# Kernel optimization log

Hardware: AMD Instinct MI355X
Metric: run time of the kernel (lower is better)

The kernel has to match this reference:

```python
import jax, jax.numpy as jnp
import numpy as np

B, T, D, H, S, Ms = 16, 512, 64, 128, 100, 20  # batch, time, input, controller, slots, slot width


def setup_inputs() -> dict:
    key = jax.random.key(0)
    ks = jax.random.split(key, 12)
    rn = lambda k, shape, s=0.08: (jax.random.normal(k, shape, dtype=jnp.float32) * s)
    inp = {}
    inp["inputs"] = jax.random.normal(ks[0], (B, T, D), dtype=jnp.float32)
    inp["memory"] = jax.random.normal(ks[1], (S, Ms), dtype=jnp.float32)
    # Keras LSTM params (gate order i, f, c, o)
    inp["lstm_kernel"] = rn(ks[2], (D, 4 * H))
    inp["lstm_rkernel"] = rn(ks[3], (H, 4 * H))
    inp["lstm_bias"] = jnp.zeros((4 * H,), jnp.float32)
    # 2 read heads: key Dense(H -> Ms)
    inp["read_Wk"] = rn(ks[4], (2, H, Ms)); inp["read_bk"] = jnp.zeros((2, Ms), jnp.float32)
    # 2 write heads: key / erase(sigmoid) / add Dense(H -> Ms)
    inp["write_Wk"] = rn(ks[5], (2, H, Ms)); inp["write_bk"] = jnp.zeros((2, Ms), jnp.float32)
    inp["write_We"] = rn(ks[6], (2, H, Ms)); inp["write_be"] = jnp.zeros((2, Ms), jnp.float32)
    inp["write_Wa"] = rn(ks[7], (2, H, Ms)); inp["write_ba"] = jnp.zeros((2, Ms), jnp.float32)
    return inp


def _lstm(x, Wk, Rk, b):
    # x: [B,T,D] -> h_seq: [B,T,H]; Keras gate order i,f,c,o
    xw = jnp.einsum('btd,dh->bth', x, Wk) + b  # precompute input projection
    h0 = jnp.zeros((x.shape[0], Rk.shape[0]), x.dtype)
    c0 = jnp.zeros_like(h0)

    def step(carry, xt):
        h, c = carry
        z = xt + h @ Rk  # [B,4H]
        i, f, g, o = jnp.split(z, 4, axis=-1)
        i = jax.nn.sigmoid(i); f = jax.nn.sigmoid(f)
        g = jnp.tanh(g); o = jax.nn.sigmoid(o)
        c = f * c + i * g
        h = o * jnp.tanh(c)
        return (h, c), h

    _, hs = jax.lax.scan(step, (h0, c0), jnp.swapaxes(xw, 0, 1))
    return jnp.swapaxes(hs, 0, 1)


def _l2n(x):
    # tf.nn.l2_normalize semantics with epsilon 1e-12
    return x / jnp.sqrt(jnp.maximum(jnp.sum(x * x, axis=-1, keepdims=True), 1e-12))


def _neg_cos(a, b):
    # tf.keras.losses.cosine_similarity returns NEGATIVE cosine
    return -jnp.sum(_l2n(a) * _l2n(b), axis=-1)


def reference(inputs, memory, lstm_kernel, lstm_rkernel, lstm_bias,
              read_Wk, read_bk, write_Wk, write_bk,
              write_We, write_be, write_Wa, write_ba):
    ctrl = _lstm(inputs, lstm_kernel, lstm_rkernel, lstm_bias)  # [B,T,H]

    # content-addressable reads (on pre-write memory, as in original)
    reads = []
    for i in range(2):
        k = jax.nn.softmax(jnp.einsum('bth,hm->btm', ctrl, read_Wk[i]) + read_bk[i], axis=-1)
        sim = _neg_cos(k[:, :, None, :], memory[None, None, :, :])  # [B,T,S]
        w = jax.nn.softmax(sim, axis=-1)
        reads.append(jnp.einsum('bts,sm->btm', w, memory))

    # content-addressable erase/add writes, applied per (batch, time) position
    mem = memory[None, None, :, :]  # broadcast to [B,T,S,Ms] lazily
    for i in range(2):
        k = jax.nn.softmax(jnp.einsum('bth,hm->btm', ctrl, write_Wk[i]) + write_bk[i], axis=-1)
        sim = _neg_cos(k[:, :, None, :], mem)  # [B,T,S]
        w = jax.nn.softmax(sim, axis=-1)
        e = jax.nn.sigmoid(jnp.einsum('bth,hm->btm', ctrl, write_We[i]) + write_be[i])
        a = jnp.einsum('bth,hm->btm', ctrl, write_Wa[i]) + write_ba[i]
        mem = (1.0 - w[..., None] * e[:, :, None, :]) * mem + w[..., None] * a[:, :, None, :]

    out = jnp.concatenate([ctrl] + reads, axis=-1)  # [B,T,H+2*Ms]
    return out, mem
```

## Files before the change

### kernel.cpp

```cpp
#include <hip/hip_runtime.h>
#include <hip/hip_bf16.h>

#define BB 16
#define TT 512
#define DD 64
#define HH 128
#define SS 100
#define MSZ 20
#define NROW (BB*TT)
#define FOURH 512

typedef __attribute__((ext_vector_type(8))) short bh8;
typedef __attribute__((ext_vector_type(4))) float fv4;

__device__ __forceinline__ float frcp(float x){ return __builtin_amdgcn_rcpf(x); }
__device__ __forceinline__ float sigmoidf_(float x){
    return frcp(1.0f + __expf(-x));
}
__device__ __forceinline__ float tanhf_(float x){
    float t = __expf(2.0f * x);
    return 1.0f - 2.0f * frcp(t + 1.0f);
}
__device__ __forceinline__ unsigned short f2bf(float f){
    __hip_bfloat16 h = __float2bfloat16(f);
    union { __hip_bfloat16 b; unsigned short u; } cv; cv.b = h;
    return cv.u;
}

__device__ __forceinline__ void lds_sync(){
    asm volatile("s_waitcnt lgkmcnt(0)" ::: "memory");
    __builtin_amdgcn_s_barrier();
    __builtin_amdgcn_sched_barrier(0);
}

__global__ __launch_bounds__(512) void k_xw(const float* __restrict__ inp,
        const float* __restrict__ Wk, const float* __restrict__ bias,
        float* __restrict__ xw){
    __shared__ float in_s[8 * DD];
    int tid = threadIdx.x;
    int r0 = blockIdx.x * 8;
    in_s[tid] = inp[(size_t)r0 * DD + tid];
    __syncthreads();
    int j = tid;
    int n = j & 127, g = j >> 7;
    float wreg[DD];
    #pragma unroll
    for (int d = 0; d < DD; ++d) wreg[d] = Wk[d * FOURH + j];
    float bv = bias[j];
    const float4* in4 = reinterpret_cast<const float4*>(in_s);
    #pragma unroll
    for (int r = 0; r < 8; ++r){
        float acc = bv;
        #pragma unroll
        for (int q = 0; q < DD/4; ++q){
            float4 iv = in4[r*(DD/4) + q];
            acc = fmaf(iv.x, wreg[4*q+0], acc);
            acc = fmaf(iv.y, wreg[4*q+1], acc);
            acc = fmaf(iv.z, wreg[4*q+2], acc);
            acc = fmaf(iv.w, wreg[4*q+3], acc);
        }
        xw[(size_t)(r0 + r) * FOURH + n*4 + g] = acc;
    }
}

__global__ __launch_bounds__(512, 2) void k_scan(const float* __restrict__ xw,
        const float* __restrict__ Rk, float* __restrict__ ctrl){
    __shared__ __align__(16) unsigned short hbuf0[HH];
    __shared__ __align__(16) unsigned short hbuf1[HH];
    const int tid = threadIdx.x;
    const int b  = blockIdx.x;
    const int w  = tid >> 6;
    const int l  = tid & 63;
    const int q  = l >> 4;
    const int lo = l & 15;
    if (tid < HH){ hbuf0[tid] = 0; hbuf1[tid] = 0; }
    bh8 bf[4][4];
    #pragma unroll
    for (int Ti = 0; Ti < 4; ++Ti){
        const int col = Ti*128 + w*16 + lo;
        #pragma unroll
        for (int kk = 0; kk < 4; ++kk){
            union { unsigned short us[8]; bh8 v; } u;
            #pragma unroll
            for (int j = 0; j < 8; ++j)
                u.us[j] = f2bf(Rk[(size_t)(kk*32 + q*8 + j)*FOURH + col]);
            bf[Ti][kk] = u.v;
        }
    }
    const bool upd = (q == 0);
    const bool rdh = (lo == 0);
    const int  n   = w*16 + lo;
    const float4* xb4 = reinterpret_cast<const float4*>(xw) + (size_t)b*TT*HH + n;
    float* cptr = ctrl + (size_t)b*TT*HH + n;
    float c0 = 0.0f;
    float4 x0 = {0,0,0,0}, x1 = {0,0,0,0}, xp0 = {0,0,0,0}, xp1 = {0,0,0,0};
    if (upd){ x0 = xb4[0]; x1 = xb4[(size_t)HH]; }
    union AU { uint4 u; bh8 v; };
    AU a0, a1, a2, a3;
    a0.u = make_uint4(0u,0u,0u,0u); a1.u = a0.u; a2.u = a0.u; a3.u = a0.u;
    const fv4 zz = {0.f, 0.f, 0.f, 0.f};
    __syncthreads();

#define MFMA16() \
        fv4 z0 = __builtin_amdgcn_mfma_f32_16x16x32_bf16(a0.v, bf[0][0], zz, 0,0,0); \
        fv4 z1 = __builtin_amdgcn_mfma_f32_16x16x32_bf16(a0.v, bf[1][0], zz, 0,0,0); \
        fv4 z2 = __builtin_amdgcn_mfma_f32_16x16x32_bf16(a0.v, bf[2][0], zz, 0,0,0); \
        fv4 z3 = __builtin_amdgcn_mfma_f32_16x16x32_bf16(a0.v, bf[3][0], zz, 0,0,0); \
        z0 = __builtin_amdgcn_mfma_f32_16x16x32_bf16(a1.v, bf[0][1], z0, 0,0,0); \
        z1 = __builtin_amdgcn_mfma_f32_16x16x32_bf16(a1.v, bf[1][1], z1, 0,0,0); \
        z2 = __builtin_amdgcn_mfma_f32_16x16x32_bf16(a1.v, bf[2][1], z2, 0,0,0); \
        z3 = __builtin_amdgcn_mfma_f32_16x16x32_bf16(a1.v, bf[3][1], z3, 0,0,0); \
        z0 = __builtin_amdgcn_mfma_f32_16x16x32_bf16(a2.v, bf[0][2], z0, 0,0,0); \
        z1 = __builtin_amdgcn_mfma_f32_16x16x32_bf16(a2.v, bf[1][2], z1, 0,0,0); \
        z2 = __builtin_amdgcn_mfma_f32_16x16x32_bf16(a2.v, bf[2][2], z2, 0,0,0); \
        z3 = __builtin_amdgcn_mfma_f32_16x16x32_bf16(a2.v, bf[3][2], z3, 0,0,0); \
        z0 = __builtin_amdgcn_mfma_f32_16x16x32_bf16(a3.v, bf[0][3], z0, 0,0,0); \
        z1 = __builtin_amdgcn_mfma_f32_16x16x32_bf16(a3.v, bf[1][3], z1, 0,0,0); \
        z2 = __builtin_amdgcn_mfma_f32_16x16x32_bf16(a3.v, bf[2][3], z2, 0,0,0); \
        z3 = __builtin_amdgcn_mfma_f32_16x16x32_bf16(a3.v, bf[3][3], z3, 0,0,0);

    for (int t = 0; t < TT; t += 2){
        if (rdh){
            const uint4* hr = reinterpret_cast<const uint4*>(hbuf0);
            a0.u = hr[q]; a1.u = hr[q+4]; a2.u = hr[q+8]; a3.u = hr[q+12];
        }
        {
            const int tn = (t+2 < TT) ? t+2 : TT-1;
            if (upd) xp0 = xb4[(size_t)tn * HH];
        }
        {
            MFMA16();
            if (upd){
                float ig = sigmoidf_(z0[0] + x0.x);
                float fg = sigmoidf_(z1[0] + x0.y);
                float gg = tanhf_   (z2[0] + x0.z);
                float og = sigmoidf_(z3[0] + x0.w);
                c0 = fg * c0 + ig * gg;
                float h = og * tanhf_(c0);
                cptr[(size_t)t * HH] = h;
                hbuf1[n] = f2bf(h);
            }
        }
        lds_sync();
        if (rdh){
            const uint4* hr = reinterpret_cast<const uint4*>(hbuf1);
            a0.u = hr[q]; a1.u = hr[q+4]; a2.u = hr[q+8]; a3.u = hr[q+12];
        }
        {
            const int tn = (t+3 < TT) ? t+3 : TT-1;
            if (upd) xp1 = xb4[(size_t)tn * HH];
        }
        {
            MFMA16();
            if (upd){
                float ig = sigmoidf_(z0[0] + x1.x);
                float fg = sigmoidf_(z1[0] + x1.y);
                float gg = tanhf_   (z2[0] + x1.z);
                float og = sigmoidf_(z3[0] + x1.w);
                c0 = fg * c0 + ig * gg;
                float h = og * tanhf_(c0);
                cptr[(size_t)(t+1) * HH] = h;
                hbuf0[n] = f2bf(h);
            }
        }
        x0 = xp0; x1 = xp1;
        lds_sync();
    }
#undef MFMA16
}

__device__ __forceinline__ float blocksum128(float v, float* red){
    #pragma unroll
    for (int o = 1; o < 64; o <<= 1) v += __shfl_xor(v, o, 64);
    int tid = threadIdx.x;
    if ((tid & 63) == 0) red[tid >> 6] = v;
    __syncthreads();
    float s = red[0] + red[1];
    __syncthreads();
    return s;
}

__global__ __launch_bounds__(128) void k_heads(const float* __restrict__ ctrl,
        const float* __restrict__ memory,
        const float* __restrict__ rWk, const float* __restrict__ rbk,
        const float* __restrict__ wWk, const float* __restrict__ wbk,
        const float* __restrict__ wWe, const float* __restrict__ wbe,
        const float* __restrict__ wWa, const float* __restrict__ wba,
        float* __restrict__ out, float* __restrict__ outmem){
    __shared__ float mem0[SS * MSZ];
    __shared__ float cs[HH];
    __shared__ float rn[SS];
    __shared__ float khat[4][MSZ];
    __shared__ float ea[4][MSZ];
    __shared__ float wrd[2][SS];
    __shared__ float red[2];
    __shared__ float pz[160];
    int tid = threadIdx.x;
    int bt = blockIdx.x;
    for (int idx = tid; idx < SS * MSZ; idx += 128) mem0[idx] = memory[idx];
    if (tid < HH){
        float v = ctrl[(size_t)bt * HH + tid];
        cs[tid] = v;
        out[(size_t)bt * 168 + tid] = v;
    }
    __syncthreads();
    if (tid < SS){
        float s2 = 0.0f;
        #pragma unroll
        for (int m = 0; m < MSZ; ++m){ float v = mem0[tid*MSZ + m]; s2 = fmaf(v, v, s2); }
        rn[tid] = rsqrtf(fmaxf(s2, 1e-12f));
    }
    for (int j = tid; j < 160; j += 128){
        int p = j / MSZ, m = j % MSZ;
        const float* Wp; const float* bp;
        switch (p){
            case 0:  Wp = rWk;            bp = rbk;        break;
            case 1:  Wp = rWk + HH*MSZ;   bp = rbk + MSZ;  break;
            case 2:  Wp = wWk;            bp = wbk;        break;
            case 3:  Wp = wWk + HH*MSZ;   bp = wbk + MSZ;  break;
            case 4:  Wp = wWe;            bp = wbe;        break;
            case 5:  Wp = wWe + HH*MSZ;   bp = wbe + MSZ;  break;
            case 6:  Wp = wWa;            bp = wba;        break;
            default: Wp = wWa + HH*MSZ;   bp = wba + MSZ;  break;
        }
        float acc = bp[m];
        const float* wcol = Wp + m;
        #pragma unroll 16
        for (int k = 0; k < HH; ++k)
            acc = fmaf(cs[k], wcol[k*MSZ], acc);
        pz[j] = acc;
    }
    __syncthreads();
    {
        int g = tid >> 5, lm = tid & 31;
        float z = (lm < MSZ) ? pz[g*MSZ + lm] : 0.0f;
        float e = (lm < MSZ) ? __expf(z) : 0.0f;
        float ssum = e;
        #pragma unroll
        for (int o = 1; o < 32; o <<= 1) ssum += __shfl_xor(ssum, o, 32);
        float kv = e / ssum;
        float qs = kv * kv;
        #pragma unroll
        for (int o = 1; o < 32; o <<= 1) qs += __shfl_xor(qs, o, 32);
        float kn = kv * rsqrtf(fmaxf(qs, 1e-12f));
        if (lm < MSZ) khat[g][lm] = kn;
        float z2 = (lm < MSZ) ? pz[80 + g*MSZ + lm] : 0.0f;
        float v2 = (g < 2) ? sigmoidf_(z2) : z2;
        if (lm < MSZ) ea[g][lm] = v2;
    }
    __syncthreads();
    bool act = tid < SS;
    int s = tid;
    float d0 = 0.f, d1 = 0.f, dw = 0.f;
    if (act){
        #pragma unroll
        for (int m = 0; m < MSZ; ++m){
            float mv = mem0[s*MSZ + m];
            d0 = fmaf(khat[0][m], mv, d0);
            d1 = fmaf(khat[1][m], mv, d1);
            dw = fmaf(khat[2][m], mv, dw);
        }
    }
    float rns = act ? rn[s] : 0.0f;
    float e0 = act ? __expf(-rns * d0) : 0.0f;
    float e1 = act ? __expf(-rns * d1) : 0.0f;
    float ew = act ? __expf(-rns * dw) : 0.0f;
    float sum0 = blocksum128(e0, red);
    float sum1 = blocksum128(e1, red);
    float sumw = blocksum128(ew, red);
    if (act){ wrd[0][s] = e0 / sum0; wrd[1][s] = e1 / sum1; }
    float w0 = ew / sumw;
    float m1[MSZ];
    float n1 = 0.f, dkw = 0.f;
    if (act){
        #pragma unroll
        for (int m = 0; m < MSZ; ++m){
            float mv = mem0[s*MSZ + m];
            float v = fmaf(-w0 * ea[0][m], mv, mv);
            v = fmaf(w0, ea[2][m], v);
            m1[m] = v;
            n1 = fmaf(v, v, n1);
            dkw = fmaf(khat[3][m], v, dkw);
        }
    }
    float rn1 = rsqrtf(fmaxf(n1, 1e-12f));
    float e1w = act ? __expf(-rn1 * dkw) : 0.0f;
    float sum1w = blocksum128(e1w, red);
    float w1 = e1w / sum1w;
    if (act){
        float buf[MSZ];
        #pragma unroll
        for (int m = 0; m < MSZ; ++m){
            float v = m1[m];
            float v2 = fmaf(-w1 * ea[1][m], v, v);
            v2 = fmaf(w1, ea[3][m], v2);
            buf[m] = v2;
        }
        float4* dst = reinterpret_cast<float4*>(outmem + ((size_t)bt * SS + s) * MSZ);
        #pragma unroll
        for (int q = 0; q < MSZ/4; ++q)
            dst[q] = make_float4(buf[4*q], buf[4*q+1], buf[4*q+2], buf[4*q+3]);
    }
    __syncthreads();
    if (tid < 2 * MSZ){
        int hd = tid / MSZ, m = tid % MSZ;
        float acc = 0.0f;
        for (int s2 = 0; s2 < SS; ++s2)
            acc = fmaf(wrd[hd][s2], mem0[s2*MSZ + m], acc);
        out[(size_t)bt * 168 + 128 + hd*MSZ + m] = acc;
    }
}

extern "C" void kernel_launch(void* const* d_in, const int* in_sizes, int n_in,
                              void* d_out, int out_size, void* d_ws, size_t ws_size,
                              hipStream_t stream){
    const float* inputs = (const float*)d_in[0];
    const float* memory = (const float*)d_in[1];
    const float* Wk     = (const float*)d_in[2];
    const float* Rk     = (const float*)d_in[3];
    const float* bias   = (const float*)d_in[4];
    const float* rWk    = (const float*)d_in[5];
    const float* rbk    = (const float*)d_in[6];
    const float* wWk    = (const float*)d_in[7];
    const float* wbk    = (const float*)d_in[8];
    const float* wWe    = (const float*)d_in[9];
    const float* wbe    = (const float*)d_in[10];
    const float* wWa    = (const float*)d_in[11];
    const float* wba    = (const float*)d_in[12];

    float* out    = (float*)d_out;
    float* outmem = out + (size_t)NROW * 168;
    float* xw   = outmem;
    float* ctrl = (float*)d_ws;

    k_xw   <<<NROW/8, 512, 0, stream>>>(inputs, Wk, bias, xw);
    k_scan <<<BB,     512, 0, stream>>>(xw, Rk, ctrl);
    k_heads<<<NROW,   128, 0, stream>>>(ctrl, memory,
                                        rWk, rbk, wWk, wbk, wWe, wbe, wWa, wba,
                                        out, outmem);
}
```

Before: 304.3 us.

## Fuse LSTM scan and memory heads into one persistent kernel with flag-based overlap

Adds a merged kernel. Its first 16 blocks run the LSTM scan, write ctrl straight into the output rows, and publish per-batch progress watermarks with release atomics every 16 steps. The remaining 240 blocks spin on those watermarks and compute the read/write heads for four rows at a time, so head work overlaps the serial recurrence instead of waiting for it to finish. The new path relies on all 256 blocks being co-resident, since heads blocks busy-wait, and on the workspace being large enough to hold xw and the flags. If the workspace is too small, it falls back to the old three-kernel path.

```diff
diff --git a/kernel.cpp b/kernel.cpp
--- a/kernel.cpp
+++ b/kernel.cpp
@@ -63,12 +63,11 @@
     }
 }
 
-__global__ __launch_bounds__(512, 2) void k_scan(const float* __restrict__ xw,
-        const float* __restrict__ Rk, float* __restrict__ ctrl){
-    __shared__ __align__(16) unsigned short hbuf0[HH];
-    __shared__ __align__(16) unsigned short hbuf1[HH];
-    const int tid = threadIdx.x;
-    const int b  = blockIdx.x;
+template<int CTRL_STRIDE>
+__device__ __forceinline__ void scan_body(const float* __restrict__ xw,
+        const float* __restrict__ Rk, float* __restrict__ ctrl,
+        unsigned int* wm, unsigned short* hbuf0, unsigned short* hbuf1,
+        int b, int tid){
     const int w  = tid >> 6;
     const int l  = tid & 63;
     const int q  = l >> 4;
@@ -91,7 +90,7 @@
     const bool rdh = (lo == 0);
     const int  n   = w*16 + lo;
     const float4* xb4 = reinterpret_cast<const float4*>(xw) + (size_t)b*TT*HH + n;
-    float* cptr = ctrl + (size_t)b*TT*HH + n;
+    float* cptr = ctrl + (size_t)b*TT*CTRL_STRIDE + n;
     float c0 = 0.0f;
     float4 x0 = {0,0,0,0}, x1 = {0,0,0,0}, xp0 = {0,0,0,0}, xp1 = {0,0,0,0};
     if (upd){ x0 = xb4[0]; x1 = xb4[(size_t)HH]; }
@@ -137,7 +136,7 @@
                 float og = sigmoidf_(z3[0] + x0.w);
                 c0 = fg * c0 + ig * gg;
                 float h = og * tanhf_(c0);
-                cptr[(size_t)t * HH] = h;
+                cptr[(size_t)t * CTRL_STRIDE] = h;
                 hbuf1[n] = f2bf(h);
             }
         }
@@ -159,14 +158,27 @@
                 float og = sigmoidf_(z3[0] + x1.w);
                 c0 = fg * c0 + ig * gg;
                 float h = og * tanhf_(c0);
-                cptr[(size_t)(t+1) * HH] = h;
+                cptr[(size_t)(t+1) * CTRL_STRIDE] = h;
                 hbuf0[n] = f2bf(h);
             }
         }
         x0 = xp0; x1 = xp1;
         lds_sync();
+        if (wm && ((t & 15) == 14)){
+            __syncthreads();
+            if (tid == 0)
+                __hip_atomic_store(&wm[b], (unsigned)(t+2),
+                                   __ATOMIC_RELEASE, __HIP_MEMORY_SCOPE_AGENT);
+        }
     }
 #undef MFMA16
+}
+
+__global__ __launch_bounds__(512, 2) void k_scan(const float* __restrict__ xw,
+        const float* __restrict__ Rk, float* __restrict__ ctrl){
+    __shared__ __align__(16) unsigned short hbuf0[HH];
+    __shared__ __align__(16) unsigned short hbuf1[HH];
+    scan_body<HH>(xw, Rk, ctrl, nullptr, hbuf0, hbuf1, blockIdx.x, threadIdx.x);
 }
 
 __device__ __forceinline__ float blocksum128(float v, float* red){
@@ -311,6 +323,177 @@
     }
 }
 
+__device__ __forceinline__ float bsum_slot(float v, float* red2){
+    #pragma unroll
+    for (int o = 1; o < 64; o <<= 1) v += __shfl_xor(v, o, 64);
+    int tid = threadIdx.x;
+    if ((tid & 63) == 0) red2[(tid >> 6) & 1] = v;
+    __syncthreads();
+    float s = red2[0] + red2[1];
+    __syncthreads();
+    return s;
+}
+
+__global__ __launch_bounds__(512, 2) void k_mega(const float* __restrict__ xw,
+        const float* __restrict__ Rk, const float* __restrict__ memory,
+        const float* __restrict__ rWk, const float* __restrict__ rbk,
+        const float* __restrict__ wWk, const float* __restrict__ wbk,
+        const float* __restrict__ wWe, const float* __restrict__ wbe,
+        const float* __restrict__ wWa, const float* __restrict__ wba,
+        float* __restrict__ out, float* __restrict__ outmem,
+        unsigned int* wm){
+    __shared__ __align__(16) unsigned short hbuf0[HH];
+    __shared__ __align__(16) unsigned short hbuf1[HH];
+    __shared__ float mem0[SS * MSZ];
+    __shared__ float rn_s[SS];
+    __shared__ float cs4[4][HH];
+    __shared__ float pz4[4][160];
+    __shared__ float kh4[4][4][MSZ];
+    __shared__ float ea4[4][4][MSZ];
+    __shared__ float wr4[4][2][SS];
+    __shared__ float rd4[4][2];
+    const int tid = threadIdx.x;
+    if (blockIdx.x < BB){
+        scan_body<168>(xw, Rk, out, wm, hbuf0, hbuf1, blockIdx.x, tid);
+        return;
+    }
+    for (int idx = tid; idx < SS * MSZ; idx += 512) mem0[idx] = memory[idx];
+    __syncthreads();
+    if (tid < SS){
+        float s2 = 0.0f;
+        #pragma unroll
+        for (int m = 0; m < MSZ; ++m){ float v = mem0[tid*MSZ + m]; s2 = fmaf(v, v, s2); }
+        rn_s[tid] = rsqrtf(fmaxf(s2, 1e-12f));
+    }
+    __syncthreads();
+    const int t128 = tid & 127;
+    const int slot = tid >> 7;
+    const int cb   = blockIdx.x - BB;
+    float* red2 = rd4[slot];
+    for (int sweep = 0; sweep < 9; ++sweep){
+        const int it = sweep*960 + cb*4 + slot;
+        const bool valid = (it < NROW);
+        const int bb = it & 15;
+        const int tt = it >> 4;
+        const size_t row = valid ? ((size_t)bb*TT + tt) : 0;
+        if (tid == 0){
+            #pragma unroll
+            for (int s4 = 0; s4 < 4; ++s4){
+                const int it2 = sweep*960 + cb*4 + s4;
+                if (it2 < NROW){
+                    const int b2 = it2 & 15, t2 = it2 >> 4;
+                    while ((int)__hip_atomic_load(&wm[b2], __ATOMIC_ACQUIRE,
+                                                  __HIP_MEMORY_SCOPE_AGENT) <= t2)
+                        __builtin_amdgcn_s_sleep(2);
+                }
+            }
+        }
+        __syncthreads();
+        cs4[slot][t128] = valid ? out[row*168 + t128] : 0.0f;
+        __syncthreads();
+        for (int j = t128; j < 160; j += 128){
+            int p = j / MSZ, m = j % MSZ;
+            const float* Wp; const float* bp;
+            switch (p){
+                case 0:  Wp = rWk;            bp = rbk;        break;
+                case 1:  Wp = rWk + HH*MSZ;   bp = rbk + MSZ;  break;
+                case 2:  Wp = wWk;            bp = wbk;        break;
+                case 3:  Wp = wWk + HH*MSZ;   bp = wbk + MSZ;  break;
+                case 4:  Wp = wWe;            bp = wbe;        break;
+                case 5:  Wp = wWe + HH*MSZ;   bp = wbe + MSZ;  break;
+                case 6:  Wp = wWa;            bp = wba;        break;
+                default: Wp = wWa + HH*MSZ;   bp = wba + MSZ;  break;
+            }
+            float acc = bp[m];
+            const float* wcol = Wp + m;
+            #pragma unroll 16
+            for (int k = 0; k < HH; ++k)
+                acc = fmaf(cs4[slot][k], wcol[k*MSZ], acc);
+            pz4[slot][j] = acc;
+        }
+        __syncthreads();
+        {
+            int g = t128 >> 5, lm = t128 & 31;
+            float z = (lm < MSZ) ? pz4[slot][g*MSZ + lm] : 0.0f;
+            float e = (lm < MSZ) ? __expf(z) : 0.0f;
+            float ssum = e;
+            #pragma unroll
+            for (int o = 1; o < 32; o <<= 1) ssum += __shfl_xor(ssum, o, 32);
+            float kv = e / ssum;
+            float qs = kv * kv;
+            #pragma unroll
+            for (int o = 1; o < 32; o <<= 1) qs += __shfl_xor(qs, o, 32);
+            float kn = kv * rsqrtf(fmaxf(qs, 1e-12f));
+            if (lm < MSZ) kh4[slot][g][lm] = kn;
+            float z2 = (lm < MSZ) ? pz4[slot][80 + g*MSZ + lm] : 0.0f;
+            float v2 = (g < 2) ? sigmoidf_(z2) : z2;
+            if (lm < MSZ) ea4[slot][g][lm] = v2;
+        }
+        __syncthreads();
+        bool act = t128 < SS;
+        int s = t128;
+        float d0 = 0.f, d1 = 0.f, dw = 0.f;
+        if (act){
+            #pragma unroll
+            for (int m = 0; m < MSZ; ++m){
+                float mv = mem0[s*MSZ + m];
+                d0 = fmaf(kh4[slot][0][m], mv, d0);
+                d1 = fmaf(kh4[slot][1][m], mv, d1);
+                dw = fmaf(kh4[slot][2][m], mv, dw);
+            }
+        }
+        float rns = act ? rn_s[s] : 0.0f;
+        float e0 = act ? __expf(-rns * d0) : 0.0f;
+        float e1 = act ? __expf(-rns * d1) : 0.0f;
+        float ew = act ? __expf(-rns * dw) : 0.0f;
+        float sum0 = bsum_slot(e0, red2);
+        float sum1 = bsum_slot(e1, red2);
+        float sumw = bsum_slot(ew, red2);
+        if (act){ wr4[slot][0][s] = e0 / sum0; wr4[slot][1][s] = e1 / sum1; }
+        float w0 = ew / sumw;
+        float m1[MSZ];
+        float n1 = 0.f, dkw = 0.f;
+        if (act){
+            #pragma unroll
+            for (int m = 0; m < MSZ; ++m){
+                float mv = mem0[s*MSZ + m];
+                float v = fmaf(-w0 * ea4[slot][0][m], mv, mv);
+                v = fmaf(w0, ea4[slot][2][m], v);
+                m1[m] = v;
+                n1 = fmaf(v, v, n1);
+                dkw = fmaf(kh4[slot][3][m], v, dkw);
+            }
+        }
+        float rn1 = rsqrtf(fmaxf(n1, 1e-12f));
+        float e1w = act ? __expf(-rn1 * dkw) : 0.0f;
+        float sum1w = bsum_slot(e1w, red2);
+        float w1 = e1w / sum1w;
+        if (act && valid){
+            float buf[MSZ];
+            #pragma unroll
+            for (int m = 0; m < MSZ; ++m){
+                float v = m1[m];
+                float v2 = fmaf(-w1 * ea4[slot][1][m], v, v);
+                v2 = fmaf(w1, ea4[slot][3][m], v2);
+                buf[m] = v2;
+            }
+            float4* dst = reinterpret_cast<float4*>(outmem + (row*SS + s)*MSZ);
+            #pragma unroll
+            for (int q = 0; q < MSZ/4; ++q)
+                dst[q] = make_float4(buf[4*q], buf[4*q+1], buf[4*q+2], buf[4*q+3]);
+        }
+        __syncthreads();
+        if (t128 < 2*MSZ && valid){
+            int hd = t128 / MSZ, m = t128 % MSZ;
+            float acc = 0.0f;
+            for (int s2 = 0; s2 < SS; ++s2)
+                acc = fmaf(wr4[slot][hd][s2], mem0[s2*MSZ + m], acc);
+            out[row*168 + 128 + hd*MSZ + m] = acc;
+        }
+        __syncthreads();
+    }
+}
+
 extern "C" void kernel_launch(void* const* d_in, const int* in_sizes, int n_in,
                               void* d_out, int out_size, void* d_ws, size_t ws_size,
                               hipStream_t stream){
@@ -330,12 +513,23 @@
 
     float* out    = (float*)d_out;
     float* outmem = out + (size_t)NROW * 168;
-    float* xw   = outmem;
-    float* ctrl = (float*)d_ws;
-
-    k_xw   <<<NROW/8, 512, 0, stream>>>(inputs, Wk, bias, xw);
-    k_scan <<<BB,     512, 0, stream>>>(xw, Rk, ctrl);
-    k_heads<<<NROW,   128, 0, stream>>>(ctrl, memory,
-                                        rWk, rbk, wWk, wbk, wWe, wbe, wWa, wba,
-                                        out, outmem);
-}
+    const size_t XW_BYTES = (size_t)NROW * FOURH * sizeof(float);
+
+    if (ws_size >= XW_BYTES + 256){
+        float* xw = (float*)d_ws;
+        unsigned int* wm = (unsigned int*)((char*)d_ws + XW_BYTES);
+        hipMemsetAsync(wm, 0, 64, stream);
+        k_xw  <<<NROW/8, 512, 0, stream>>>(inputs, Wk, bias, xw);
+        k_mega<<<256,    512, 0, stream>>>(xw, Rk, memory,
+                                           rWk, rbk, wWk, wbk, wWe, wbe, wWa, wba,
+                                           out, outmem, wm);
+    } else {
+        float* xw   = outmem;
+        float* ctrl = (float*)d_ws;
+        k_xw   <<<NROW/8, 512, 0, stream>>>(inputs, Wk, bias, xw);
+        k_scan <<<BB,     512, 0, stream>>>(xw, Rk, ctrl);
+        k_heads<<<NROW,   128, 0, stream>>>(ctrl, memory,
+                                            rWk, rbk, wWk, wbk, wWe, wbe, wWa, wba,
+                                            out, outmem);
+    }
+}
```

Measured after the change: 486.5 us. 1.6x slower.

## Replace MFMA recurrent matvec with per-thread fp16 dot2 and gate shuffles

Applied to the files above, without the earlier changes.

The LSTM scan kernel drops the bf16 MFMA-based recurrent matmul. Each thread now holds one column of the recurrent kernel as 64 packed fp16 pairs in registers and computes its gate pre-activation with fdot2 over h read from LDS. The four gates of each hidden unit are combined with lane shuffles, and h is stored in fp16 instead of bf16. This aims to cut the per-step latency of MFMA chains and the LDS broadcast pattern, at the cost of heavy register use (launch bounds lowered to one block per CU) and fp16 range/precision differences.

```diff
diff --git a/kernel.cpp b/kernel.cpp
--- a/kernel.cpp
+++ b/kernel.cpp
@@ -10,8 +10,14 @@
 #define NROW (BB*TT)
 #define FOURH 512
 
-typedef __attribute__((ext_vector_type(8))) short bh8;
-typedef __attribute__((ext_vector_type(4))) float fv4;
+typedef _Float16 hf2 __attribute__((ext_vector_type(2)));
+
+#if __has_builtin(__builtin_amdgcn_fdot2)
+  #define FDOT2(a, b, c) __builtin_amdgcn_fdot2((a), (b), (c), false)
+#else
+  #define FDOT2(a, b, c) fmaf((float)(a).x, (float)(b).x, \
+                          fmaf((float)(a).y, (float)(b).y, (c)))
+#endif
 
 __device__ __forceinline__ float frcp(float x){ return __builtin_amdgcn_rcpf(x); }
 __device__ __forceinline__ float sigmoidf_(float x){
@@ -20,11 +26,6 @@
 __device__ __forceinline__ float tanhf_(float x){
     float t = __expf(2.0f * x);
     return 1.0f - 2.0f * frcp(t + 1.0f);
-}
-__device__ __forceinline__ unsigned short f2bf(float f){
-    __hip_bfloat16 h = __float2bfloat16(f);
-    union { __hip_bfloat16 b; unsigned short u; } cv; cv.b = h;
-    return cv.u;
 }
 
 __device__ __forceinline__ void lds_sync(){
@@ -63,110 +64,71 @@
     }
 }
 
-__global__ __launch_bounds__(512, 2) void k_scan(const float* __restrict__ xw,
+__global__ __launch_bounds__(512, 1) void k_scan(const float* __restrict__ xw,
         const float* __restrict__ Rk, float* __restrict__ ctrl){
-    __shared__ __align__(16) unsigned short hbuf0[HH];
-    __shared__ __align__(16) unsigned short hbuf1[HH];
+    __shared__ __align__(16) _Float16 hbuf0[HH];
+    __shared__ __align__(16) _Float16 hbuf1[HH];
     const int tid = threadIdx.x;
-    const int b  = blockIdx.x;
-    const int w  = tid >> 6;
-    const int l  = tid & 63;
-    const int q  = l >> 4;
-    const int lo = l & 15;
-    if (tid < HH){ hbuf0[tid] = 0; hbuf1[tid] = 0; }
-    bh8 bf[4][4];
+    const int b = blockIdx.x;
+    const int n = tid >> 2;
+    const int g = tid & 3;
+    const int col = g * HH + n;
+    if (tid < HH){ hbuf0[tid] = (_Float16)0.f; hbuf1[tid] = (_Float16)0.f; }
+    hf2 rk[64];
     #pragma unroll
-    for (int Ti = 0; Ti < 4; ++Ti){
-        const int col = Ti*128 + w*16 + lo;
-        #pragma unroll
-        for (int kk = 0; kk < 4; ++kk){
-            union { unsigned short us[8]; bh8 v; } u;
-            #pragma unroll
-            for (int j = 0; j < 8; ++j)
-                u.us[j] = f2bf(Rk[(size_t)(kk*32 + q*8 + j)*FOURH + col]);
-            bf[Ti][kk] = u.v;
-        }
-    }
-    const bool upd = (q == 0);
-    const bool rdh = (lo == 0);
-    const int  n   = w*16 + lo;
-    const float4* xb4 = reinterpret_cast<const float4*>(xw) + (size_t)b*TT*HH + n;
-    float* cptr = ctrl + (size_t)b*TT*HH + n;
-    float c0 = 0.0f;
-    float4 x0 = {0,0,0,0}, x1 = {0,0,0,0}, xp0 = {0,0,0,0}, xp1 = {0,0,0,0};
-    if (upd){ x0 = xb4[0]; x1 = xb4[(size_t)HH]; }
-    union AU { uint4 u; bh8 v; };
-    AU a0, a1, a2, a3;
-    a0.u = make_uint4(0u,0u,0u,0u); a1.u = a0.u; a2.u = a0.u; a3.u = a0.u;
-    const fv4 zz = {0.f, 0.f, 0.f, 0.f};
-    __syncthreads();
-
-#define MFMA16() \
-        fv4 z0 = __builtin_amdgcn_mfma_f32_16x16x32_bf16(a0.v, bf[0][0], zz, 0,0,0); \
-        fv4 z1 = __builtin_amdgcn_mfma_f32_16x16x32_bf16(a0.v, bf[1][0], zz, 0,0,0); \
-        fv4 z2 = __builtin_amdgcn_mfma_f32_16x16x32_bf16(a0.v, bf[2][0], zz, 0,0,0); \
-        fv4 z3 = __builtin_amdgcn_mfma_f32_16x16x32_bf16(a0.v, bf[3][0], zz, 0,0,0); \
-        z0 = __builtin_amdgcn_mfma_f32_16x16x32_bf16(a1.v, bf[0][1], z0, 0,0,0); \
-        z1 = __builtin_amdgcn_mfma_f32_16x16x32_bf16(a1.v, bf[1][1], z1, 0,0,0); \
-        z2 = __builtin_amdgcn_mfma_f32_16x16x32_bf16(a1.v, bf[2][1], z2, 0,0,0); \
-        z3 = __builtin_amdgcn_mfma_f32_16x16x32_bf16(a1.v, bf[3][1], z3, 0,0,0); \
-        z0 = __builtin_amdgcn_mfma_f32_16x16x32_bf16(a2.v, bf[0][2], z0, 0,0,0); \
-        z1 = __builtin_amdgcn_mfma_f32_16x16x32_bf16(a2.v, bf[1][2], z1, 0,0,0); \
-        z2 = __builtin_amdgcn_mfma_f32_16x16x32_bf16(a2.v, bf[2][2], z2, 0,0,0); \
-        z3 = __builtin_amdgcn_mfma_f32_16x16x32_bf16(a2.v, bf[3][2], z3, 0,0,0); \
-        z0 = __builtin_amdgcn_mfma_f32_16x16x32_bf16(a3.v, bf[0][3], z0, 0,0,0); \
-        z1 = __builtin_amdgcn_mfma_f32_16x16x32_bf16(a3.v, bf[1][3], z1, 0,0,0); \
-        z2 = __builtin_amdgcn_mfma_f32_16x16x32_bf16(a3.v, bf[2][3], z2, 0,0,0); \
-        z3 = __builtin_amdgcn_mfma_f32_16x16x32_bf16(a3.v, bf[3][3], z3, 0,0,0);
+    for (int i = 0; i < 64; ++i){
+        hf2 v;
+        v.x = (_Float16)Rk[(size_t)(2*i    ) * FOURH + col];
+        v.y = (_Float16)Rk[(size_t)(2*i + 1) * FOURH + col];
+        rk[i] = v;
+    }
+    const float* xp = xw + (size_t)b * TT * FOURH + tid;
+    float* cp = ctrl + (size_t)b * TT * HH + n;
+    float c = 0.0f;
+    float x0 = xp[0];
+    float x1 = xp[FOURH];
+    union HU { uint4 u; hf2 h[4]; };
+    __syncthreads();
+
+#define DOT_STEP(HRD, HWR, XV, TOFF, TPRE, XNEW) { \
+        float a0 = 0.f, a1 = 0.f, a2 = 0.f, a3 = 0.f; \
+        const uint4* hr = reinterpret_cast<const uint4*>(HRD); \
+        _Pragma("unroll") \
+        for (int m = 0; m < 16; ++m){ \
+            HU hu; hu.u = hr[m]; \
+            a0 = FDOT2(hu.h[0], rk[4*m+0], a0); \
+            a1 = FDOT2(hu.h[1], rk[4*m+1], a1); \
+            a2 = FDOT2(hu.h[2], rk[4*m+2], a2); \
+            a3 = FDOT2(hu.h[3], rk[4*m+3], a3); \
+        } \
+        XNEW = xp[(size_t)(TPRE) * FOURH]; \
+        float z = ((a0 + a1) + (a2 + a3)) + (XV); \
+        float zx1 = __shfl_xor(z, 1); \
+        float zx2 = __shfl_xor(z, 2); \
+        float zx3 = __shfl_xor(zx1, 2); \
+        float ig = sigmoidf_(z);       \
+        float fg = sigmoidf_(zx1); \
+        float gg = tanhf_   (zx2); \
+        float og = sigmoidf_(zx3); \
+        c = fg * c + ig * gg; \
+        float h = og * tanhf_(c); \
+        if (g == 0){ \
+            cp[(size_t)(TOFF) * HH] = h; \
+            (HWR)[n] = (_Float16)h; \
+        } \
+        (XV) = XNEW; \
+    }
 
     for (int t = 0; t < TT; t += 2){
-        if (rdh){
-            const uint4* hr = reinterpret_cast<const uint4*>(hbuf0);
-            a0.u = hr[q]; a1.u = hr[q+4]; a2.u = hr[q+8]; a3.u = hr[q+12];
-        }
-        {
-            const int tn = (t+2 < TT) ? t+2 : TT-1;
-            if (upd) xp0 = xb4[(size_t)tn * HH];
-        }
-        {
-            MFMA16();
-            if (upd){
-                float ig = sigmoidf_(z0[0] + x0.x);
-                float fg = sigmoidf_(z1[0] + x0.y);
-                float gg = tanhf_   (z2[0] + x0.z);
-                float og = sigmoidf_(z3[0] + x0.w);
-                c0 = fg * c0 + ig * gg;
-                float h = og * tanhf_(c0);
-                cptr[(size_t)t * HH] = h;
-                hbuf1[n] = f2bf(h);
-            }
-        }
+        float xn0, xn1;
+        const int tp0 = (t+2 < TT) ? t+2 : TT-1;
+        const int tp1 = (t+3 < TT) ? t+3 : TT-1;
+        DOT_STEP(hbuf0, hbuf1, x0, t,   tp0, xn0);
         lds_sync();
-        if (rdh){
-            const uint4* hr = reinterpret_cast<const uint4*>(hbuf1);
-            a0.u = hr[q]; a1.u = hr[q+4]; a2.u = hr[q+8]; a3.u = hr[q+12];
-        }
-        {
-            const int tn = (t+3 < TT) ? t+3 : TT-1;
-            if (upd) xp1 = xb4[(size_t)tn * HH];
-        }
-        {
-            MFMA16();
-            if (upd){
-                float ig = sigmoidf_(z0[0] + x1.x);
-                float fg = sigmoidf_(z1[0] + x1.y);
-                float gg = tanhf_   (z2[0] + x1.z);
-                float og = sigmoidf_(z3[0] + x1.w);
-                c0 = fg * c0 + ig * gg;
-                float h = og * tanhf_(c0);
-                cptr[(size_t)(t+1) * HH] = h;
-                hbuf0[n] = f2bf(h);
-            }
-        }
-        x0 = xp0; x1 = xp1;
+        DOT_STEP(hbuf1, hbuf0, x1, t+1, tp1, xn1);
         lds_sync();
     }
-#undef MFMA16
+#undef DOT_STEP
 }
 
 __device__ __forceinline__ float blocksum128(float v, float* red){
```

Result: slower. 393.6 us (+29.3%).
